# Kernel tuning notes

Hardware: AMD Instinct MI355X
Metric: run time of the kernel (lower is better)

Reference implementation:

```python
import jax, jax.numpy as jnp
from jax import lax
import numpy as np

VTH = 1.0  # config['v_threshold']

@jax.custom_vjp
def mg_spike(x):
    # forward of MultiGaussianSurrogate: Heaviside
    return (x > 0).astype(x.dtype)

def _mg_fwd(x):
    return mg_spike(x), x

def _mg_bwd(x, g):
    lens, scale, height, gamma = 0.5, 6.0, 0.15, 0.5
    def gaussian(v, mu, sigma):
        return jnp.exp(-(v - mu) ** 2 / (2.0 * sigma ** 2)) / jnp.sqrt(2.0 * jnp.pi) / sigma
    temp = (gaussian(x, 0.0, lens) * (1.0 + height)
            - gaussian(x, lens, scale * lens) * height
            - gaussian(x, -lens, scale * lens) * height)
    return (g * temp * gamma,)

mg_spike.defvjp(_mg_fwd, _mg_bwd)

def setup_inputs():
    key = jax.random.key(0)
    ks = jax.random.split(key, 6)
    B, T, D, H, O = 256, 250, 700, 1024, 35
    x = jax.random.normal(ks[0], (B, T, D), dtype=jnp.float32)
    W_dense = jax.random.normal(ks[1], (D, H), dtype=jnp.float32) / np.sqrt(D).astype(np.float32)
    b_dense = jnp.zeros((H,), dtype=jnp.float32)
    W_out = jax.random.normal(ks[2], (H, O), dtype=jnp.float32) / np.sqrt(H).astype(np.float32)
    b_out = jnp.zeros((O,), dtype=jnp.float32)
    tau_m = jax.random.uniform(ks[3], (H,), dtype=jnp.float32, minval=0.0, maxval=4.0)
    mem0 = jax.random.uniform(ks[4], (B, H), dtype=jnp.float32)
    spike0 = jax.random.uniform(ks[5], (B, H), dtype=jnp.float32)
    return {"x": x, "W_dense": W_dense, "b_dense": b_dense,
            "W_out": W_out, "b_out": b_out, "tau_m": tau_m,
            "mem0": mem0, "spike0": spike0}

def reference(x, W_dense, b_dense, W_out, b_out, tau_m, mem0, spike0):
    B, T, D = x.shape
    O = W_out.shape[1]
    alpha = jax.nn.sigmoid(tau_m)  # [H], constant over time
    # batch the input projection once: [B,T,H] -> scan over T
    d_all = jnp.einsum('btd,dh->bth', x, W_dense) + b_dense
    d_all = jnp.swapaxes(d_all, 0, 1)  # [T,B,H]

    def step(carry, inp):
        mem, spike, acc = carry
        d_input, i = inp
        mem = mem * alpha + (1.0 - alpha) * d_input - VTH * spike
        spike = mg_spike(mem - VTH)
        probs = jax.nn.softmax(spike @ W_out + b_out, axis=1)  # [B,O]
        acc = acc + jnp.where(i > 10, probs, jnp.zeros_like(probs))
        return (mem, spike, acc), None

    acc0 = jnp.zeros((B, O), dtype=x.dtype)
    (_, _, out), _ = lax.scan(step, (mem0, spike0, acc0), (d_all, jnp.arange(T)))
    return out
```

## Files before the change

### kernel.cpp

```cpp
#include <hip/hip_runtime.h>
#include <cstdint>
#include <cstddef>

#define B_ 256
#define T_ 250
#define D_ 700
#define KP 704
#define H_ 1024
#define O_ 35
#define NT 22
#define MPAD 256

typedef __attribute__((ext_vector_type(8))) short s16x8;
typedef __attribute__((ext_vector_type(4))) float fx4;

__device__ __forceinline__ unsigned short f2bf(float v) {
    union { float f; unsigned int u; } a; a.f = v;
    unsigned int r = a.u + 0x7FFFu + ((a.u >> 16) & 1u);
    return (unsigned short)(r >> 16);
}

__device__ __forceinline__ void glds16(const unsigned short* g, void* l) {
    __builtin_amdgcn_global_load_lds(
        (const __attribute__((address_space(1))) unsigned int*)(const void*)g,
        (__attribute__((address_space(3))) unsigned int*)l, 16, 0, 0);
}

__global__ __launch_bounds__(256)
void convW(const float* __restrict__ Wd, unsigned short* __restrict__ WhT,
           unsigned short* __restrict__ WlT)
{
    __shared__ float tile[32][33];
    const int tx = threadIdx.x, ty = threadIdx.y;
    const int bx = blockIdx.x, by = blockIdx.y;
#pragma unroll
    for (int i = 0; i < 4; ++i) {
        int k = by * 32 + ty + i * 8;
        int n = bx * 32 + tx;
        tile[ty + i * 8][tx] = (k < D_) ? Wd[(size_t)k * H_ + n] : 0.f;
    }
    __syncthreads();
#pragma unroll
    for (int i = 0; i < 4; ++i) {
        int n = bx * 32 + ty + i * 8;
        int k = by * 32 + tx;
        float v = tile[tx][ty + i * 8];
        unsigned short h = f2bf(v);
        union { unsigned int u; float f; } hf; hf.u = ((unsigned int)h) << 16;
        unsigned short lo = f2bf(v - hf.f);
        WhT[(size_t)n * KP + k] = h;
        WlT[(size_t)n * KP + k] = lo;
    }
}

__global__ __launch_bounds__(256)
void convX(const float* __restrict__ X, unsigned short* __restrict__ xh,
           unsigned short* __restrict__ xl)
{
    int idx = blockIdx.x * 256 + threadIdx.x;
    if (idx >= B_ * T_ * 88) return;
    int m = idx / 88, s = idx - m * 88;
    int k = s * 8;
    int b = m / T_, tt = m - b * T_;
    const float* row = X + (size_t)m * D_;
    float4 vA = *reinterpret_cast<const float4*>(row + k);
    float4 vB = (k + 4 < D_) ? *reinterpret_cast<const float4*>(row + k + 4)
                             : make_float4(0.f, 0.f, 0.f, 0.f);
    float v[8] = {vA.x, vA.y, vA.z, vA.w, vB.x, vB.y, vB.z, vB.w};
    unsigned int hw[4], lw[4];
#pragma unroll
    for (int j = 0; j < 4; ++j) {
        unsigned short h0 = f2bf(v[2 * j]), h1 = f2bf(v[2 * j + 1]);
        union { unsigned int u; float f; } a0, a1;
        a0.u = ((unsigned int)h0) << 16; a1.u = ((unsigned int)h1) << 16;
        unsigned short l0 = f2bf(v[2 * j] - a0.f), l1 = f2bf(v[2 * j + 1] - a1.f);
        hw[j] = (unsigned int)h0 | ((unsigned int)h1 << 16);
        lw[j] = (unsigned int)l0 | ((unsigned int)l1 << 16);
    }
    size_t drow = (size_t)(b * MPAD + tt) * KP + k;
    *reinterpret_cast<uint4*>(xh + drow) = make_uint4(hw[0], hw[1], hw[2], hw[3]);
    *reinterpret_cast<uint4*>(xl + drow) = make_uint4(lw[0], lw[1], lw[2], lw[3]);
}

__global__ __launch_bounds__(512, 1)
void gemm1(const unsigned short* __restrict__ Ahp, const unsigned short* __restrict__ Alp,
           const unsigned short* __restrict__ Bhp, const unsigned short* __restrict__ Blp,
           const float* __restrict__ bias, const float* __restrict__ tau,
           const float* __restrict__ mem0, const float* __restrict__ spk0,
           unsigned long long* __restrict__ bits)
{
    extern __shared__ char smem[];
    const int tid = threadIdx.x;
    const int l = tid & 63, w = tid >> 6;
    const int wm = w >> 2, wn = w & 3;

    const int nwg = gridDim.x, orig = blockIdx.x;
    const int xcd = orig & 7, idx = orig >> 3;
    const int q = nwg >> 3, r = nwg & 7;
    const int swz = (xcd < r ? xcd * (q + 1) : r * (q + 1) + (xcd - r) * q) + idx;
    const int by = swz >> 2, bx = swz & 3;
    const int m0 = by * MPAD, n0 = bx * 256;

    const int rr = tid >> 2, ss = tid & 3;
    const int sw8 = ((ss ^ ((rr >> 1) & 3)) << 3);
    const int offA = (m0 + rr) * KP + sw8;
    const int offB = (n0 + rr) * KP + sw8;
    const int wbase = w * 1024;

    const int ra0 = wm * 128 + (l & 15);
    const int rb0 = wn * 64 + (l & 15);
    const int aHb = ra0 * 64 + (((l >> 4) ^ ((ra0 >> 1) & 3)) << 4);
    const int bHb = rb0 * 64 + (((l >> 4) ^ ((rb0 >> 1) & 3)) << 4);

    fx4 acc[8][4];
#pragma unroll
    for (int i = 0; i < 8; ++i)
#pragma unroll
        for (int j = 0; j < 4; ++j) acc[i][j] = (fx4)0.f;

    auto stageA = [&](int buf, int t) {
        char* base = smem + buf * 32768 + wbase;
        const int k = t * 32;
        glds16(Ahp + offA + k, base);
        glds16(Ahp + offA + 128 * KP + k, base + 8192);
        glds16(Alp + offA + k, base + 16384);
        glds16(Alp + offA + 128 * KP + k, base + 24576);
    };
    auto stageB = [&](int bufB, int t) {
        char* base = smem + 65536 + bufB * 32768 + wbase;
        const int k = t * 32;
        glds16(Bhp + offB + k, base);
        glds16(Bhp + offB + 128 * KP + k, base + 8192);
        glds16(Blp + offB + k, base + 16384);
        glds16(Blp + offB + 128 * KP + k, base + 24576);
    };

    stageB(0, 0);
    stageB(1, 1);
    stageA(0, 0);
    asm volatile("s_waitcnt vmcnt(0)" ::: "memory");
    __builtin_amdgcn_s_barrier();

    for (int t = 0; t < NT; ++t) {
        const char* ab = smem + (t & 1) * 32768;
        const char* bb = smem + 65536 + (t % 3) * 32768;
        s16x8 ah0[4], al0[4], ah1[4], al1[4], bh[4], bl[4];

        if (t + 1 < NT) {
            asm volatile("s_waitcnt vmcnt(4)" ::: "memory");
        } else {
            asm volatile("s_waitcnt vmcnt(0)" ::: "memory");
        }
        __builtin_amdgcn_sched_barrier(0);

#pragma unroll
        for (int f = 0; f < 4; ++f) {
            ah0[f] = *(const s16x8*)(ab + aHb + f * 1024);
            bh[f]  = *(const s16x8*)(bb + bHb + f * 1024);
        }
        if (t + 1 < NT) stageA((t + 1) & 1, t + 1);

#pragma unroll
        for (int f = 0; f < 4; ++f) {
            al0[f] = *(const s16x8*)(ab + 16384 + aHb + f * 1024);
            bl[f]  = *(const s16x8*)(bb + 16384 + bHb + f * 1024);
        }
        __builtin_amdgcn_s_setprio(1);
#pragma unroll
        for (int fm = 0; fm < 4; ++fm)
#pragma unroll
            for (int fn = 0; fn < 4; ++fn)
                acc[fm][fn] = __builtin_amdgcn_mfma_f32_16x16x32_bf16(ah0[fm], bh[fn], acc[fm][fn], 0, 0, 0);
        __builtin_amdgcn_s_setprio(0);

#pragma unroll
        for (int f = 0; f < 4; ++f) {
            ah1[f] = *(const s16x8*)(ab + aHb + 4096 + f * 1024);
            al1[f] = *(const s16x8*)(ab + 16384 + aHb + 4096 + f * 1024);
        }
        __builtin_amdgcn_s_setprio(1);
#pragma unroll
        for (int fm = 0; fm < 4; ++fm)
#pragma unroll
            for (int fn = 0; fn < 4; ++fn) {
                acc[fm][fn] = __builtin_amdgcn_mfma_f32_16x16x32_bf16(ah0[fm], bl[fn], acc[fm][fn], 0, 0, 0);
                acc[fm][fn] = __builtin_amdgcn_mfma_f32_16x16x32_bf16(al0[fm], bh[fn], acc[fm][fn], 0, 0, 0);
            }
        __builtin_amdgcn_s_setprio(0);
        __builtin_amdgcn_sched_barrier(0);

        if (t + 2 < NT) stageB((t + 2) % 3, t + 2);

        __builtin_amdgcn_s_setprio(1);
#pragma unroll
        for (int fm = 0; fm < 4; ++fm)
#pragma unroll
            for (int fn = 0; fn < 4; ++fn)
                acc[fm + 4][fn] = __builtin_amdgcn_mfma_f32_16x16x32_bf16(ah1[fm], bh[fn], acc[fm + 4][fn], 0, 0, 0);
        __builtin_amdgcn_s_setprio(0);

        __builtin_amdgcn_s_setprio(1);
#pragma unroll
        for (int fm = 0; fm < 4; ++fm)
#pragma unroll
            for (int fn = 0; fn < 4; ++fn) {
                acc[fm + 4][fn] = __builtin_amdgcn_mfma_f32_16x16x32_bf16(ah1[fm], bl[fn], acc[fm + 4][fn], 0, 0, 0);
                acc[fm + 4][fn] = __builtin_amdgcn_mfma_f32_16x16x32_bf16(al1[fm], bh[fn], acc[fm + 4][fn], 0, 0, 0);
            }
        __builtin_amdgcn_s_setprio(0);
        __builtin_amdgcn_sched_barrier(0);
        __builtin_amdgcn_s_barrier();
    }

    float bv[4];
#pragma unroll
    for (int fn = 0; fn < 4; ++fn) bv[fn] = bias[n0 + wn * 64 + fn * 16 + (l & 15)];

    float* dl = (float*)smem;
    const int bb2 = by;
    const int lane = tid & 63;

    float memv = 0.f, spkv = 0.f, alh = 0.f, omh = 0.f;
    unsigned long long* bp = nullptr;
    if (tid < 256) {
        const int h = n0 + tid;
        alh = 1.f / (1.f + expf(-tau[h]));
        omh = 1.f - alh;
        memv = mem0[bb2 * H_ + h];
        spkv = spk0[bb2 * H_ + h];
        bp = bits + (((size_t)bb2 * T_) << 4) + (h >> 6);
    }

#pragma unroll 1
    for (int ck = 0; ck < 2; ++ck) {
        __syncthreads();
        if (wm == ck) {
            const int colb = wn * 64;
#pragma unroll
            for (int fm = 0; fm < 8; ++fm) {
#pragma unroll
                for (int fn = 0; fn < 4; ++fn) {
                    int col = colb + fn * 16 + (l & 15);
#pragma unroll
                    for (int rg = 0; rg < 4; ++rg) {
                        int row = fm * 16 + (l >> 4) * 4 + rg;
                        dl[row * 256 + (col ^ (((row >> 2) & 1) << 4))] = acc[fm][fn][rg] + bv[fn];
                    }
                }
            }
        }
        __syncthreads();
        if (tid < 256) {
            const int nsteps = ck ? (T_ - 128) : 128;
            const int tbase = ck * 128;
            int ttl = 0;
            for (; ttl + 8 <= nsteps; ttl += 8) {
                float dr[8];
#pragma unroll
                for (int j = 0; j < 8; ++j) {
                    int rj = ttl + j;
                    dr[j] = dl[rj * 256 + (tid ^ (((rj >> 2) & 1) << 4))];
                }
#pragma unroll
                for (int j = 0; j < 8; ++j) {
                    memv = memv * alh + omh * dr[j] - spkv;
                    bool fire = (memv - 1.f) > 0.f;
                    spkv = fire ? 1.f : 0.f;
                    unsigned long long msk = __ballot(fire);
                    if (lane == 0) bp[(size_t)(tbase + ttl + j) << 4] = msk;
                }
            }
            for (; ttl < nsteps; ++ttl) {
                float d = dl[ttl * 256 + (tid ^ (((ttl >> 2) & 1) << 4))];
                memv = memv * alh + omh * d - spkv;
                bool fire = (memv - 1.f) > 0.f;
                spkv = fire ? 1.f : 0.f;
                unsigned long long msk = __ballot(fire);
                if (lane == 0) bp[(size_t)(tbase + ttl) << 4] = msk;
            }
        }
    }
}

__global__ __launch_bounds__(1024)
void out_fused(const unsigned long long* __restrict__ bits,
               const float* __restrict__ Wo, const float* __restrict__ bo,
               float* __restrict__ out)
{
    __shared__ float sp[239][37];
    __shared__ float part[64][36];
    const int tid = threadIdx.x;
    const int b = blockIdx.x;
    const int rrow = tid >> 2;
    const int q = tid & 3;

    if (rrow < 239) {
        const int t = rrow + 11;
        float lg[35];
#pragma unroll
        for (int o = 0; o < 35; ++o) lg[o] = (q == 0) ? bo[o] : 0.f;
        const unsigned long long* bp = bits + ((size_t)(b * T_ + t) << 4) + q * 4;
#pragma unroll
        for (int w2 = 0; w2 < 4; ++w2) {
            unsigned long long wb = bp[w2];
            const float* wbase = Wo + (size_t)((q * 4 + w2) * 64) * O_;
            while (wb) {
                int i = __builtin_ctzll(wb);
                wb &= wb - 1;
                const float* wr = wbase + i * O_;
#pragma unroll
                for (int o = 0; o < 35; ++o) lg[o] += wr[o];
            }
        }
#pragma unroll
        for (int o = 0; o < 35; ++o) lg[o] += __shfl_xor(lg[o], 1);
#pragma unroll
        for (int o = 0; o < 35; ++o) lg[o] += __shfl_xor(lg[o], 2);
        float mx = lg[0];
#pragma unroll
        for (int o = 1; o < 35; ++o) mx = fmaxf(mx, lg[o]);
        float sum = 0.f;
#pragma unroll
        for (int o = 0; o < 35; ++o) { lg[o] = expf(lg[o] - mx); sum += lg[o]; }
        float inv = 1.f / sum;
#pragma unroll
        for (int o = 0; o < 35; ++o) if (o / 9 == q) sp[rrow][o] = lg[o] * inv;
    }
    __syncthreads();
    if (tid < 256) {
        const int rl = tid >> 2, qq = tid & 3;
        float a9[9];
#pragma unroll
        for (int j = 0; j < 9; ++j) a9[j] = 0.f;
        for (int c = 0; c < 239; c += 64) {
            int i = c + rl;
            if (i < 239) {
#pragma unroll
                for (int j = 0; j < 9; ++j) if (j < 8 || qq < 3) a9[j] += sp[i][qq * 9 + j];
            }
        }
#pragma unroll
        for (int j = 0; j < 9; ++j) if (j < 8 || qq < 3) part[rl][qq * 9 + j] = a9[j];
    }
    __syncthreads();
    if (tid < 35) {
        float a = 0.f;
        for (int rr = 0; rr < 64; ++rr) a += part[rr][tid];
        out[b * O_ + tid] = a;
    }
}

extern "C" void kernel_launch(void* const* d_in, const int* in_sizes, int n_in,
                              void* d_out, int out_size, void* d_ws, size_t ws_size,
                              hipStream_t stream) {
    const float* x    = (const float*)d_in[0];
    const float* Wd   = (const float*)d_in[1];
    const float* bd   = (const float*)d_in[2];
    const float* Wo   = (const float*)d_in[3];
    const float* bo   = (const float*)d_in[4];
    const float* tau  = (const float*)d_in[5];
    const float* mem0 = (const float*)d_in[6];
    const float* spk0 = (const float*)d_in[7];
    float* out = (float*)d_out;

    char* ws = (char*)d_ws;
    size_t off = 0;
    auto take = [&](size_t bytes) -> void* {
        void* p = ws + off;
        off = (off + bytes + 255) & ~(size_t)255;
        return p;
    };

    unsigned long long* bits = (unsigned long long*)take((size_t)B_ * T_ * 16 * 8);
    unsigned short* WhT = (unsigned short*)take((size_t)H_ * KP * 2);
    unsigned short* WlT = (unsigned short*)take((size_t)H_ * KP * 2);
    unsigned short* xh = (unsigned short*)take((size_t)B_ * MPAD * KP * 2);
    unsigned short* xl = (unsigned short*)take((size_t)B_ * MPAD * KP * 2);

    (void)hipFuncSetAttribute((const void*)gemm1,
                              hipFuncAttributeMaxDynamicSharedMemorySize, 163840);

    convW<<<dim3(32, 22), dim3(32, 8), 0, stream>>>(Wd, WhT, WlT);
    convX<<<(B_ * T_ * 88 + 255) / 256, 256, 0, stream>>>(x, xh, xl);
    gemm1<<<B_ * 4, 512, 163840, stream>>>(xh, xl, WhT, WlT, bd, tau, mem0, spk0, bits);
    out_fused<<<B_, 1024, 0, stream>>>(bits, Wo, bo, out);
}
```

Baseline: 326.4 us.

## Fuse fp32-to-bf16 hi/lo split of X into GEMM A-tile loads

Removes the separate convX kernel and its padded bf16 hi/lo copies of X. The GEMM now streams raw fp32 rows of X straight into LDS and splits them into bf16 hi/lo fragments in registers before the MFMAs. A small zero buffer stands in for the K tail past D, and rows beyond T are clamped. This saves a full read-write round trip of the large input, but it doubles the A bytes per tile and adds conversion ALU work inside the GEMM inner loop.

Result: slower. 397.3 us (+21.7%).

```diff
diff --git a/kernel.cpp b/kernel.cpp
--- a/kernel.cpp
+++ b/kernel.cpp
@@ -20,19 +20,35 @@
     return (unsigned short)(r >> 16);
 }
 
-__device__ __forceinline__ void glds16(const unsigned short* g, void* l) {
+__device__ __forceinline__ void glds16(const void* g, void* l) {
     __builtin_amdgcn_global_load_lds(
-        (const __attribute__((address_space(1))) unsigned int*)(const void*)g,
+        (const __attribute__((address_space(1))) unsigned int*)g,
         (__attribute__((address_space(3))) unsigned int*)l, 16, 0, 0);
+}
+
+__device__ __forceinline__ void split8(float4 va, float4 vb, s16x8& hi8, s16x8& lo8) {
+    float v[8] = {va.x, va.y, va.z, va.w, vb.x, vb.y, vb.z, vb.w};
+    union { unsigned int u[4]; s16x8 s; } Hu, Lu;
+#pragma unroll
+    for (int j = 0; j < 4; ++j) {
+        unsigned short h0 = f2bf(v[2 * j]), h1 = f2bf(v[2 * j + 1]);
+        union { unsigned int u; float f; } a0, a1;
+        a0.u = ((unsigned int)h0) << 16; a1.u = ((unsigned int)h1) << 16;
+        unsigned short l0 = f2bf(v[2 * j] - a0.f), l1 = f2bf(v[2 * j + 1] - a1.f);
+        Hu.u[j] = (unsigned int)h0 | ((unsigned int)h1 << 16);
+        Lu.u[j] = (unsigned int)l0 | ((unsigned int)l1 << 16);
+    }
+    hi8 = Hu.s; lo8 = Lu.s;
 }
 
 __global__ __launch_bounds__(256)
 void convW(const float* __restrict__ Wd, unsigned short* __restrict__ WhT,
-           unsigned short* __restrict__ WlT)
+           unsigned short* __restrict__ WlT, float* __restrict__ zbuf)
 {
     __shared__ float tile[32][33];
     const int tx = threadIdx.x, ty = threadIdx.y;
     const int bx = blockIdx.x, by = blockIdx.y;
+    if (bx == 0 && by == 0 && tx < 4 && ty == 0) zbuf[tx] = 0.f;
 #pragma unroll
     for (int i = 0; i < 4; ++i) {
         int k = by * 32 + ty + i * 8;
@@ -53,41 +69,12 @@
     }
 }
 
-__global__ __launch_bounds__(256)
-void convX(const float* __restrict__ X, unsigned short* __restrict__ xh,
-           unsigned short* __restrict__ xl)
-{
-    int idx = blockIdx.x * 256 + threadIdx.x;
-    if (idx >= B_ * T_ * 88) return;
-    int m = idx / 88, s = idx - m * 88;
-    int k = s * 8;
-    int b = m / T_, tt = m - b * T_;
-    const float* row = X + (size_t)m * D_;
-    float4 vA = *reinterpret_cast<const float4*>(row + k);
-    float4 vB = (k + 4 < D_) ? *reinterpret_cast<const float4*>(row + k + 4)
-                             : make_float4(0.f, 0.f, 0.f, 0.f);
-    float v[8] = {vA.x, vA.y, vA.z, vA.w, vB.x, vB.y, vB.z, vB.w};
-    unsigned int hw[4], lw[4];
-#pragma unroll
-    for (int j = 0; j < 4; ++j) {
-        unsigned short h0 = f2bf(v[2 * j]), h1 = f2bf(v[2 * j + 1]);
-        union { unsigned int u; float f; } a0, a1;
-        a0.u = ((unsigned int)h0) << 16; a1.u = ((unsigned int)h1) << 16;
-        unsigned short l0 = f2bf(v[2 * j] - a0.f), l1 = f2bf(v[2 * j + 1] - a1.f);
-        hw[j] = (unsigned int)h0 | ((unsigned int)h1 << 16);
-        lw[j] = (unsigned int)l0 | ((unsigned int)l1 << 16);
-    }
-    size_t drow = (size_t)(b * MPAD + tt) * KP + k;
-    *reinterpret_cast<uint4*>(xh + drow) = make_uint4(hw[0], hw[1], hw[2], hw[3]);
-    *reinterpret_cast<uint4*>(xl + drow) = make_uint4(lw[0], lw[1], lw[2], lw[3]);
-}
-
 __global__ __launch_bounds__(512, 1)
-void gemm1(const unsigned short* __restrict__ Ahp, const unsigned short* __restrict__ Alp,
+void gemm1(const float* __restrict__ X,
            const unsigned short* __restrict__ Bhp, const unsigned short* __restrict__ Blp,
            const float* __restrict__ bias, const float* __restrict__ tau,
            const float* __restrict__ mem0, const float* __restrict__ spk0,
-           unsigned long long* __restrict__ bits)
+           unsigned long long* __restrict__ bits, const float* __restrict__ zbuf)
 {
     extern __shared__ char smem[];
     const int tid = threadIdx.x;
@@ -99,18 +86,26 @@
     const int q = nwg >> 3, r = nwg & 7;
     const int swz = (xcd < r ? xcd * (q + 1) : r * (q + 1) + (xcd - r) * q) + idx;
     const int by = swz >> 2, bx = swz & 3;
-    const int m0 = by * MPAD, n0 = bx * 256;
+    const int n0 = bx * 256;
 
     const int rr = tid >> 2, ss = tid & 3;
+    const int rrow1 = (rr + 128 <= 249) ? rr + 128 : 249;
+    const int lq0 = ss ^ ((rr >> 1) & 3);
+    const int lq1 = ss ^ ((rrow1 >> 1) & 3);
+    const float* pA0 = X + (size_t)(by * T_ + rr) * D_ + lq0 * 4;
+    const float* pA1 = X + (size_t)(by * T_ + rrow1) * D_ + lq1 * 4;
+    const bool tl0 = (lq0 == 3), tl1 = (lq1 == 3);
+
     const int sw8 = ((ss ^ ((rr >> 1) & 3)) << 3);
-    const int offA = (m0 + rr) * KP + sw8;
     const int offB = (n0 + rr) * KP + sw8;
     const int wbase = w * 1024;
 
     const int ra0 = wm * 128 + (l & 15);
     const int rb0 = wn * 64 + (l & 15);
-    const int aHb = ra0 * 64 + (((l >> 4) ^ ((ra0 >> 1) & 3)) << 4);
-    const int bHb = rb0 * 64 + (((l >> 4) ^ ((rb0 >> 1) & 3)) << 4);
+    const int swzA = (ra0 >> 1) & 3;
+    const int g = l >> 4;
+    const int aP = (g >> 1) * 16384 + ra0 * 64 + (((2 * (g & 1)) ^ swzA) << 4);
+    const int bHb = rb0 * 64 + ((g ^ ((rb0 >> 1) & 3)) << 4);
 
     fx4 acc[8][4];
 #pragma unroll
@@ -120,11 +115,13 @@
 
     auto stageA = [&](int buf, int t) {
         char* base = smem + buf * 32768 + wbase;
-        const int k = t * 32;
-        glds16(Ahp + offA + k, base);
-        glds16(Ahp + offA + 128 * KP + k, base + 8192);
-        glds16(Alp + offA + k, base + 16384);
-        glds16(Alp + offA + 128 * KP + k, base + 24576);
+        const int kf = t * 32;
+        glds16(pA0 + kf, base);
+        glds16(pA1 + kf, base + 8192);
+        const float* s2 = (t == 21 && tl0) ? zbuf : pA0 + kf + 16;
+        const float* s3 = (t == 21 && tl1) ? zbuf : pA1 + kf + 16;
+        glds16(s2, base + 16384);
+        glds16(s3, base + 24576);
     };
     auto stageB = [&](int bufB, int t) {
         char* base = smem + 65536 + bufB * 32768 + wbase;
@@ -145,6 +142,7 @@
         const char* ab = smem + (t & 1) * 32768;
         const char* bb = smem + 65536 + (t % 3) * 32768;
         s16x8 ah0[4], al0[4], ah1[4], al1[4], bh[4], bl[4];
+        float4 fa[4], fb[4];
 
         if (t + 1 < NT) {
             asm volatile("s_waitcnt vmcnt(4)" ::: "memory");
@@ -155,16 +153,20 @@
 
 #pragma unroll
         for (int f = 0; f < 4; ++f) {
-            ah0[f] = *(const s16x8*)(ab + aHb + f * 1024);
-            bh[f]  = *(const s16x8*)(bb + bHb + f * 1024);
+            int o = aP + f * 1024;
+            fa[f] = *(const float4*)(ab + o);
+            fb[f] = *(const float4*)(ab + (o ^ 16));
+            bh[f] = *(const s16x8*)(bb + bHb + f * 1024);
         }
         if (t + 1 < NT) stageA((t + 1) & 1, t + 1);
 
 #pragma unroll
-        for (int f = 0; f < 4; ++f) {
-            al0[f] = *(const s16x8*)(ab + 16384 + aHb + f * 1024);
-            bl[f]  = *(const s16x8*)(bb + 16384 + bHb + f * 1024);
-        }
+        for (int f = 0; f < 4; ++f) split8(fa[f], fb[f], ah0[f], al0[f]);
+
+#pragma unroll
+        for (int f = 0; f < 4; ++f)
+            bl[f] = *(const s16x8*)(bb + 16384 + bHb + f * 1024);
+
         __builtin_amdgcn_s_setprio(1);
 #pragma unroll
         for (int fm = 0; fm < 4; ++fm)
@@ -175,8 +177,9 @@
 
 #pragma unroll
         for (int f = 0; f < 4; ++f) {
-            ah1[f] = *(const s16x8*)(ab + aHb + 4096 + f * 1024);
-            al1[f] = *(const s16x8*)(ab + 16384 + aHb + 4096 + f * 1024);
+            int o = aP + 4096 + f * 1024;
+            fa[f] = *(const float4*)(ab + o);
+            fb[f] = *(const float4*)(ab + (o ^ 16));
         }
         __builtin_amdgcn_s_setprio(1);
 #pragma unroll
@@ -187,6 +190,9 @@
                 acc[fm][fn] = __builtin_amdgcn_mfma_f32_16x16x32_bf16(al0[fm], bh[fn], acc[fm][fn], 0, 0, 0);
             }
         __builtin_amdgcn_s_setprio(0);
+
+#pragma unroll
+        for (int f = 0; f < 4; ++f) split8(fa[f], fb[f], ah1[f], al1[f]);
         __builtin_amdgcn_sched_barrier(0);
 
         if (t + 2 < NT) stageB((t + 2) % 3, t + 2);
@@ -374,14 +380,12 @@
     unsigned long long* bits = (unsigned long long*)take((size_t)B_ * T_ * 16 * 8);
     unsigned short* WhT = (unsigned short*)take((size_t)H_ * KP * 2);
     unsigned short* WlT = (unsigned short*)take((size_t)H_ * KP * 2);
-    unsigned short* xh = (unsigned short*)take((size_t)B_ * MPAD * KP * 2);
-    unsigned short* xl = (unsigned short*)take((size_t)B_ * MPAD * KP * 2);
+    float* zbuf = (float*)take(256);
 
     (void)hipFuncSetAttribute((const void*)gemm1,
                               hipFuncAttributeMaxDynamicSharedMemorySize, 163840);
 
-    convW<<<dim3(32, 22), dim3(32, 8), 0, stream>>>(Wd, WhT, WlT);
-    convX<<<(B_ * T_ * 88 + 255) / 256, 256, 0, stream>>>(x, xh, xl);
-    gemm1<<<B_ * 4, 512, 163840, stream>>>(xh, xl, WhT, WlT, bd, tau, mem0, spk0, bits);
+    convW<<<dim3(32, 22), dim3(32, 8), 0, stream>>>(Wd, WhT, WlT, zbuf);
+    gemm1<<<B_ * 4, 512, 163840, stream>>>(x, WhT, WlT, bd, tau, mem0, spk0, bits, zbuf);
     out_fused<<<B_, 1024, 0, stream>>>(bits, Wo, bo, out);
 }
```
